# Performance work log

Hardware: AMD Instinct MI355X
Metric: run time of the kernel (lower is better)

## Reference

```python
import jax, jax.numpy as jnp
import numpy as np

WINDOW = 11
CHANNEL = 3
SIGMA = 1.5


def _gaussian_kernel():
    coords = jnp.arange(WINDOW, dtype=jnp.float32) - (WINDOW - 1) / 2.0
    g = jnp.exp(-(coords ** 2) / (2.0 * SIGMA ** 2))
    g = g / g.sum()
    k2d = g[:, None] * g[None, :]                      # (k, k)
    # depthwise kernel, OIHW with feature_group_count=C -> (C, 1, k, k)
    return jnp.tile(k2d[None, None], (CHANNEL, 1, 1, 1))


def _dwconv(x, kernel):
    pad = WINDOW // 2
    return jax.lax.conv_general_dilated(
        x, kernel, window_strides=(1, 1),
        padding=((pad, pad), (pad, pad)),
        dimension_numbers=("NCHW", "OIHW", "NCHW"),
        feature_group_count=CHANNEL)


def setup_inputs() -> dict:
    key = jax.random.key(0)
    k1, k2 = jax.random.split(key)
    B, C, H, W = 32, 3, 512, 512
    denoised = jax.random.uniform(k1, (B, C, H, W), dtype=jnp.float32)
    clean = jax.random.uniform(k2, (B, C, H, W), dtype=jnp.float32)
    return {"denoised": denoised, "clean": clean}


def reference(denoised, clean):
    kernel = _gaussian_kernel()
    img1 = jnp.clip(denoised, 0.0, 1.0)
    img2 = jnp.clip(clean, 0.0, 1.0)

    mu1 = _dwconv(img1, kernel)
    mu2 = _dwconv(img2, kernel)
    mu1_sq = mu1 * mu1
    mu2_sq = mu2 * mu2
    mu1_mu2 = mu1 * mu2
    sigma1_sq = _dwconv(img1 * img1, kernel) - mu1_sq
    sigma2_sq = _dwconv(img2 * img2, kernel) - mu2_sq
    sigma12 = _dwconv(img1 * img2, kernel) - mu1_mu2

    C1 = 0.01 ** 2
    C2 = 0.03 ** 2
    ssim_map = ((2.0 * mu1_mu2 + C1) * (2.0 * sigma12 + C2)) / (
        (mu1_sq + mu2_sq + C1) * (sigma1_sq + sigma2_sq + C2))
    return 1.0 - ssim_map.mean()
```

## Files before the change

### kernel.cpp

```cpp
#include <hip/hip_runtime.h>

#define IMG 512
#define OUT_R 16
#define OUT_C 128
#define HALO 5
#define IN_R 26
#define IN_C 138
#define CPAD 144
#define VS 152
#define NT 256
#define NSLOTS 64

typedef _Float16 f16x8 __attribute__((ext_vector_type(8)));
typedef float    f32x4 __attribute__((ext_vector_type(4)));

static constexpr float GWf[11] = {
    0.00102838f, 0.00759876f, 0.03600077f, 0.10936053f, 0.21300556f,
    0.26601170f, 0.21300556f, 0.10936053f, 0.03600077f, 0.00759876f,
    0.00102838f };

struct WTab { alignas(16) _Float16 v[4][16][8]; };
static constexpr WTab make_wtab() {
    WTab t{};
    for (int g = 0; g < 4; ++g)
        for (int j = 0; j < 16; ++j)
            for (int b = 0; b < 8; ++b) {
                const int d = 8 * g + b - j;
                t.v[g][j][b] = (d >= 0 && d <= 10) ? (_Float16)GWf[d]
                                                   : (_Float16)0.f;
            }
    return t;
}
__device__ constexpr WTab WTAB = make_wtab();

union SMem {
    _Float16 ch[4][CPAD][32];
    _Float16 vb[4][OUT_R][VS];
};
static_assert(sizeof(SMem) == 4 * CPAD * 32 * 2, "smem size");

__device__ __forceinline__ void prep_task(int task, int c0, int y0,
                                          size_t pbase,
                                          const float* __restrict__ den,
                                          const float* __restrict__ cln,
                                          SMem* sm) {
    const int rh = (task >= CPAD) ? 1 : 0;
    const int c  = task - CPAD * rh;
    const int gc = c0 - HALO + c;
    const bool colok = ((unsigned)gc < IMG) && (c < IN_C);
    union { f16x8 v8[8]; _Float16 h[64]; } st;
    const int r0 = rh * 16;
#pragma unroll
    for (int rr = 0; rr < 16; ++rr) {
        const int R  = r0 + rr;
        const int gr = y0 - HALO + R;
        float x = 0.f, y = 0.f;
        if (colok && ((unsigned)gr < IMG) && (R < IN_R)) {
            const size_t idx = pbase + (size_t)gr * IMG + gc;
            x = den[idx]; y = cln[idx];
        }
        x = fminf(fmaxf(x, 0.f), 1.f);
        y = fminf(fmaxf(y, 0.f), 1.f);
        st.h[rr]      = (_Float16)x;
        st.h[16 + rr] = (_Float16)y;
        st.h[32 + rr] = (_Float16)fmaf(x, x, y * y);
        st.h[48 + rr] = (_Float16)(x * y);
    }
    const int sw = (c >> 1) & 3;
#pragma unroll
    for (int ch = 0; ch < 4; ++ch) {
#pragma unroll
        for (int gg = 0; gg < 2; ++gg) {
            const int g = rh * 2 + gg;
            *reinterpret_cast<f16x8*>(&sm->ch[ch][c][(g ^ sw) * 8]) =
                st.v8[ch * 2 + gg];
        }
    }
}

__global__ __launch_bounds__(NT, 4)
void ssim_mfma(const float* __restrict__ den, const float* __restrict__ cln,
               double* __restrict__ slots) {
    __shared__ SMem sm;
    __shared__ float red[NT / 64];

    const int t    = threadIdx.x;
    const int lane = t & 63;
    const int w    = t >> 6;
    const int fj   = lane & 15;
    const int fg   = lane >> 4;

    const int bid = blockIdx.x;
    int vid = bid;
    if ((gridDim.x & 7) == 0) {
        const int chunk = gridDim.x >> 3;
        vid = (bid & 7) * chunk + (bid >> 3);
    }
    const int rs    = vid & 31;
    const int cs    = (vid >> 5) & 3;
    const int plane = vid >> 7;
    const int c0 = cs * OUT_C;
    const int y0 = rs * OUT_R;
    const size_t pbase = (size_t)plane * (IMG * IMG);

    const f16x8 wf = *reinterpret_cast<const f16x8*>(WTAB.v[fg][fj]);

    prep_task(t, c0, y0, pbase, den, cln, &sm);
    if (t < 2 * CPAD - NT)
        prep_task(NT + t, c0, y0, pbase, den, cln, &sm);
    __syncthreads();

    const f32x4 zero4 = {0.f, 0.f, 0.f, 0.f};
    f32x4 acc[9];
#pragma unroll
    for (int n = 0; n < 9; ++n) {
        const int tau  = 9 * w + n;
        const int tile = tau >> 2;
        const int ch   = tau & 3;
        const int colp = tile * 16 + fj;
        const f16x8 bf = *reinterpret_cast<const f16x8*>(
            &sm.ch[ch][colp][(fg ^ ((colp >> 1) & 3)) * 8]);
        acc[n] = __builtin_amdgcn_mfma_f32_16x16x32_f16(wf, bf, zero4, 0, 0, 0);
    }
    __syncthreads();
#pragma unroll
    for (int n = 0; n < 9; ++n) {
        const int tau  = 9 * w + n;
        const int tile = tau >> 2;
        const int ch   = tau & 3;
#pragma unroll
        for (int b = 0; b < 4; ++b)
            sm.vb[ch][4 * fg + b][tile * 16 + fj] = (_Float16)acc[n][b];
    }
    __syncthreads();

    float sacc = 0.f;
#pragma unroll
    for (int mt = 0; mt < 2; ++mt) {
        const int m = 2 * w + mt;
        f32x4 d[4];
#pragma unroll
        for (int ch = 0; ch < 4; ++ch) {
            const f16x8 af = *reinterpret_cast<const f16x8*>(
                &sm.vb[ch][fj][m * 16 + 8 * fg]);
            d[ch] = __builtin_amdgcn_mfma_f32_16x16x32_f16(af, wf, zero4, 0, 0, 0);
        }
#pragma unroll
        for (int b = 0; b < 4; ++b) {
            const float C1 = 1e-4f, C2 = 9e-4f;
            const float mu1 = d[0][b], mu2 = d[1][b];
            const float qb  = d[2][b], pb  = d[3][b];
            const float mu1s = mu1 * mu1, mu2s = mu2 * mu2, mu12 = mu1 * mu2;
            const float ssum = qb - mu1s - mu2s;
            const float s12  = pb - mu12;
            const float num  = fmaf(2.f, mu12, C1) * fmaf(2.f, s12, C2);
            const float dnm  = (mu1s + mu2s + C1) * (ssum + C2);
            sacc = fmaf(num, __builtin_amdgcn_rcpf(dnm), sacc);
        }
    }

#pragma unroll
    for (int off = 32; off > 0; off >>= 1)
        sacc += __shfl_down(sacc, off, 64);
    if (lane == 0) red[w] = sacc;
    __syncthreads();
    if (t == 0) {
        const float s = red[0] + red[1] + red[2] + red[3];
        atomicAdd(&slots[(size_t)(bid & (NSLOTS - 1)) * 8], (double)s);
    }
}

__global__ void ssim_finalize(const double* __restrict__ slots,
                              float* __restrict__ out, double inv_n) {
    double s = 0.0;
    for (int i = 0; i < NSLOTS; ++i) s += slots[i * 8];
    out[0] = 1.0f - (float)(s * inv_n);
}

extern "C" void kernel_launch(void* const* d_in, const int* in_sizes, int n_in,
                              void* d_out, int out_size, void* d_ws,
                              size_t ws_size, hipStream_t stream) {
    const float* den = (const float*)d_in[0];
    const float* cln = (const float*)d_in[1];
    float* out = (float*)d_out;
    double* slots = (double*)d_ws;

    hipMemsetAsync(d_ws, 0, NSLOTS * 64, stream);

    const int n = in_sizes[0];
    const int planes = n / (IMG * IMG);
    dim3 grid(planes * (IMG / OUT_R) * (IMG / OUT_C));
    ssim_mfma<<<grid, NT, 0, stream>>>(den, cln, slots);
    ssim_finalize<<<1, 1, 0, stream>>>(slots, out, 1.0 / (double)n);
}
```

Baseline: 337.3 us.

## Halve output tile width to 64 columns and raise occupancy to 8 blocks

Shrinks each block's output tile from 16x128 to 16x64 columns, which doubles the grid and cuts LDS per block. The staging work is split into four 8-row groups per column, so each thread loads fewer rows, and the reduction scratch moves into the LDS union. Launch bounds rise to 8 blocks per CU to improve latency hiding. In exchange, the halo fraction grows: input columns per output go from 138/128 to 74/64, which means more redundant global loads and vertical-pass MFMA work.

Result: faster. 273.9 us (-18.8%).

```diff
diff --git a/kernel.cpp b/kernel.cpp
--- a/kernel.cpp
+++ b/kernel.cpp
@@ -2,12 +2,13 @@
 
 #define IMG 512
 #define OUT_R 16
-#define OUT_C 128
+#define OUT_C 64
 #define HALO 5
 #define IN_R 26
-#define IN_C 138
-#define CPAD 144
-#define VS 152
+#define IN_C 74
+#define CPAD 80
+#define NVTILE 5
+#define VS 88
 #define NT 256
 #define NSLOTS 64
 
@@ -35,7 +36,7 @@
 
 union SMem {
     _Float16 ch[4][CPAD][32];
-    _Float16 vb[4][OUT_R][VS];
+    struct { _Float16 vb[4][OUT_R][VS]; float red[8]; } s;
 };
 static_assert(sizeof(SMem) == 4 * CPAD * 32 * 2, "smem size");
 
@@ -44,14 +45,14 @@
                                           const float* __restrict__ den,
                                           const float* __restrict__ cln,
                                           SMem* sm) {
-    const int rh = (task >= CPAD) ? 1 : 0;
-    const int c  = task - CPAD * rh;
+    const int c = task % CPAD;
+    const int g = task / CPAD;
     const int gc = c0 - HALO + c;
     const bool colok = ((unsigned)gc < IMG) && (c < IN_C);
-    union { f16x8 v8[8]; _Float16 h[64]; } st;
-    const int r0 = rh * 16;
+    union { f16x8 v8[4]; _Float16 h[32]; } st;
+    const int r0 = g * 8;
 #pragma unroll
-    for (int rr = 0; rr < 16; ++rr) {
+    for (int rr = 0; rr < 8; ++rr) {
         const int R  = r0 + rr;
         const int gr = y0 - HALO + R;
         float x = 0.f, y = 0.f;
@@ -62,27 +63,20 @@
         x = fminf(fmaxf(x, 0.f), 1.f);
         y = fminf(fmaxf(y, 0.f), 1.f);
         st.h[rr]      = (_Float16)x;
-        st.h[16 + rr] = (_Float16)y;
-        st.h[32 + rr] = (_Float16)fmaf(x, x, y * y);
-        st.h[48 + rr] = (_Float16)(x * y);
+        st.h[8 + rr]  = (_Float16)y;
+        st.h[16 + rr] = (_Float16)fmaf(x, x, y * y);
+        st.h[24 + rr] = (_Float16)(x * y);
     }
-    const int sw = (c >> 1) & 3;
+    const int slot = g ^ ((c >> 1) & 3);
 #pragma unroll
-    for (int ch = 0; ch < 4; ++ch) {
-#pragma unroll
-        for (int gg = 0; gg < 2; ++gg) {
-            const int g = rh * 2 + gg;
-            *reinterpret_cast<f16x8*>(&sm->ch[ch][c][(g ^ sw) * 8]) =
-                st.v8[ch * 2 + gg];
-        }
-    }
+    for (int ch = 0; ch < 4; ++ch)
+        *reinterpret_cast<f16x8*>(&sm->ch[ch][c][slot * 8]) = st.v8[ch];
 }
 
-__global__ __launch_bounds__(NT, 4)
+__global__ __launch_bounds__(NT, 8)
 void ssim_mfma(const float* __restrict__ den, const float* __restrict__ cln,
                double* __restrict__ slots) {
     __shared__ SMem sm;
-    __shared__ float red[NT / 64];
 
     const int t    = threadIdx.x;
     const int lane = t & 63;
@@ -97,8 +91,8 @@
         vid = (bid & 7) * chunk + (bid >> 3);
     }
     const int rs    = vid & 31;
-    const int cs    = (vid >> 5) & 3;
-    const int plane = vid >> 7;
+    const int cs    = (vid >> 5) & 7;
+    const int plane = vid >> 8;
     const int c0 = cs * OUT_C;
     const int y0 = rs * OUT_R;
     const size_t pbase = (size_t)plane * (IMG * IMG);
@@ -106,15 +100,15 @@
     const f16x8 wf = *reinterpret_cast<const f16x8*>(WTAB.v[fg][fj]);
 
     prep_task(t, c0, y0, pbase, den, cln, &sm);
-    if (t < 2 * CPAD - NT)
+    if (t < 4 * CPAD - NT)
         prep_task(NT + t, c0, y0, pbase, den, cln, &sm);
     __syncthreads();
 
     const f32x4 zero4 = {0.f, 0.f, 0.f, 0.f};
-    f32x4 acc[9];
+    f32x4 acc[NVTILE];
 #pragma unroll
-    for (int n = 0; n < 9; ++n) {
-        const int tau  = 9 * w + n;
+    for (int n = 0; n < NVTILE; ++n) {
+        const int tau  = NVTILE * w + n;
         const int tile = tau >> 2;
         const int ch   = tau & 3;
         const int colp = tile * 16 + fj;
@@ -124,25 +118,24 @@
     }
     __syncthreads();
 #pragma unroll
-    for (int n = 0; n < 9; ++n) {
-        const int tau  = 9 * w + n;
+    for (int n = 0; n < NVTILE; ++n) {
+        const int tau  = NVTILE * w + n;
         const int tile = tau >> 2;
         const int ch   = tau & 3;
 #pragma unroll
         for (int b = 0; b < 4; ++b)
-            sm.vb[ch][4 * fg + b][tile * 16 + fj] = (_Float16)acc[n][b];
+            sm.s.vb[ch][4 * fg + b][tile * 16 + fj] = (_Float16)acc[n][b];
     }
     __syncthreads();
 
     float sacc = 0.f;
-#pragma unroll
-    for (int mt = 0; mt < 2; ++mt) {
-        const int m = 2 * w + mt;
+    {
+        const int m = w;
         f32x4 d[4];
 #pragma unroll
         for (int ch = 0; ch < 4; ++ch) {
             const f16x8 af = *reinterpret_cast<const f16x8*>(
-                &sm.vb[ch][fj][m * 16 + 8 * fg]);
+                &sm.s.vb[ch][fj][m * 16 + 8 * fg]);
             d[ch] = __builtin_amdgcn_mfma_f32_16x16x32_f16(af, wf, zero4, 0, 0, 0);
         }
 #pragma unroll
@@ -162,10 +155,10 @@
 #pragma unroll
     for (int off = 32; off > 0; off >>= 1)
         sacc += __shfl_down(sacc, off, 64);
-    if (lane == 0) red[w] = sacc;
+    if (lane == 0) sm.s.red[w] = sacc;
     __syncthreads();
     if (t == 0) {
-        const float s = red[0] + red[1] + red[2] + red[3];
+        const float s = sm.s.red[0] + sm.s.red[1] + sm.s.red[2] + sm.s.red[3];
         atomicAdd(&slots[(size_t)(bid & (NSLOTS - 1)) * 8], (double)s);
     }
 }
```
